# Performance work log

Hardware: AMD Instinct MI355X
Metric: run time of the kernel (lower is better)

The kernel has to match this reference:

```python
import jax, jax.numpy as jnp
import numpy as np

NUM_HEADS = 4
NUM_GROUPS = 8
EPS = 1e-5


def group_norm(x, w, b):
    # x: [B, C, H, W], 8 groups, per-channel affine
    B, C, H, W = x.shape
    g = x.reshape(B, NUM_GROUPS, C // NUM_GROUPS, H, W)
    mu = g.mean(axis=(2, 3, 4), keepdims=True)
    var = g.var(axis=(2, 3, 4), keepdims=True)
    g = (g - mu) * jax.lax.rsqrt(var + EPS)
    x = g.reshape(B, C, H, W)
    return x * w[None, :, None, None] + b[None, :, None, None]


def setup_inputs() -> dict:
    key = jax.random.key(0)
    ks = jax.random.split(key, 7)
    B, C, H, W = 16, 256, 32, 32
    x = jax.random.normal(ks[0], (B, C, H, W), dtype=jnp.float32)
    norm_w = jnp.ones((C,), jnp.float32)
    norm_b = jnp.zeros((C,), jnp.float32)
    # 1x1 convs == channel matmuls; fan-in scaled init
    qkv_w = jax.random.normal(ks[1], (3 * C, C), dtype=jnp.float32) / np.sqrt(C)
    qkv_b = jnp.zeros((3 * C,), jnp.float32)
    proj_w = jax.random.normal(ks[2], (C, C), dtype=jnp.float32) / np.sqrt(C)
    proj_b = jnp.zeros((C,), jnp.float32)
    return {"x": x, "norm_w": norm_w, "norm_b": norm_b,
            "qkv_w": qkv_w, "qkv_b": qkv_b,
            "proj_w": proj_w, "proj_b": proj_b}


def reference(x, norm_w, norm_b, qkv_w, qkv_b, proj_w, proj_b):
    B, C, H, W = x.shape
    nh = NUM_HEADS
    d = C // nh
    N = H * W

    h = group_norm(x, norm_w, norm_b)
    # 1x1 conv -> channel matmul: [B, 3C, H, W]
    qkv = jnp.einsum('oc,bchw->bohw', qkv_w, h) + qkv_b[None, :, None, None]
    qkv = qkv.reshape(B, 3, nh, d, N)
    q, k, v = qkv[:, 0], qkv[:, 1], qkv[:, 2]  # [B, nh, d, N]

    scale = d ** (-0.5)
    attn = jnp.einsum('bhcn,bhcm->bhnm', q, k) * scale  # [B, nh, N, N]
    attn = jax.nn.softmax(attn, axis=-1)
    out = jnp.einsum('bhnm,bhcm->bhcn', attn, v)  # [B, nh, d, N]
    out = out.reshape(B, C, H, W)
    out = jnp.einsum('oc,bchw->bohw', proj_w, out) + proj_b[None, :, None, None]
    return x + out
```

## Files before the change

kernel.cpp:

```cpp
#include <hip/hip_runtime.h>
#include <math.h>

#define BATCH 16
#define CH 256
#define NG 8
#define NH 4
#define HD 64
#define NN 1024
#define GSZ 32
#define GELEMS (GSZ * NN)

typedef __attribute__((ext_vector_type(8))) __bf16 bf16x8;
typedef __attribute__((ext_vector_type(4))) __bf16 bf16x4;
typedef __attribute__((ext_vector_type(4))) float f32x4;

__device__ __forceinline__ unsigned short f2b(float f) {
    union { __bf16 h; unsigned short u; } c; c.h = (__bf16)f; return c.u;
}

#define MFMA(a, b, c) __builtin_amdgcn_mfma_f32_16x16x32_bf16(a, b, c, 0, 0, 0)

typedef __attribute__((address_space(1))) unsigned int ga_u32;
typedef __attribute__((address_space(3))) unsigned int ls_u32;
__device__ __forceinline__ void dma16(const void* g, void* l) {
    __builtin_amdgcn_global_load_lds((ga_u32*)g, (ls_u32*)l, 16, 0, 0);
}

__global__ __launch_bounds__(256) void prep_kernel(
    const float* __restrict__ x, const float* __restrict__ qkv_w,
    const float* __restrict__ proj_w, float* __restrict__ stats,
    unsigned short* __restrict__ wq, unsigned short* __restrict__ wp)
{
    int tid = threadIdx.x;
    if (blockIdx.x >= 128) {
        int t = (blockIdx.x - 128) * 256 + tid;
        const float* src; unsigned short* dst; size_t off;
        if (t < 24576) { src = qkv_w; dst = wq; off = (size_t)t * 8; }
        else           { src = proj_w; dst = wp; off = (size_t)(t - 24576) * 8; }
        const float4* s4 = (const float4*)(src + off);
        float4 a = s4[0], b = s4[1];
        bf16x8 pk;
        pk[0] = (__bf16)a.x; pk[1] = (__bf16)a.y; pk[2] = (__bf16)a.z; pk[3] = (__bf16)a.w;
        pk[4] = (__bf16)b.x; pk[5] = (__bf16)b.y; pk[6] = (__bf16)b.z; pk[7] = (__bf16)b.w;
        *(bf16x8*)(dst + off) = pk;
        return;
    }
    int b = blockIdx.x >> 3, g = blockIdx.x & 7;
    const float4* x4 = (const float4*)(x + ((size_t)b * CH + g * GSZ) * NN);
    float s = 0.f, ss = 0.f;
    #pragma unroll
    for (int i = 0; i < 32; ++i) {
        float4 v = x4[tid + i * 256];
        s  += v.x + v.y + v.z + v.w;
        ss += v.x * v.x + v.y * v.y + v.z * v.z + v.w * v.w;
    }
    #pragma unroll
    for (int off = 1; off < 64; off <<= 1) {
        s  += __shfl_xor(s, off);
        ss += __shfl_xor(ss, off);
    }
    __shared__ float red[8];
    int wave = tid >> 6, lane = tid & 63;
    if (lane == 0) { red[wave] = s; red[4 + wave] = ss; }
    __syncthreads();
    if (tid == 0) {
        float ts  = red[0] + red[1] + red[2] + red[3];
        float tss = red[4] + red[5] + red[6] + red[7];
        float mu  = ts * (1.f / GELEMS);
        float var = tss * (1.f / GELEMS) - mu * mu;
        stats[blockIdx.x * 2] = mu;
        stats[blockIdx.x * 2 + 1] = rsqrtf(var + 1e-5f);
    }
}

__global__ __launch_bounds__(256) void gn_apply_kernel(
    const float* __restrict__ x, const float* __restrict__ w,
    const float* __restrict__ bb, const float* __restrict__ stats,
    unsigned short* __restrict__ hT)
{
    __shared__ float Ts[64][68];
    __shared__ float wcp[256], bcp[256];
    const int b = blockIdx.y, n0 = blockIdx.x * 64;
    const int tid = threadIdx.x;
    {
        int c = tid, g = c >> 5;
        float mu = stats[(b * 8 + g) * 2], rs = stats[(b * 8 + g) * 2 + 1];
        float wc = w[c] * rs;
        wcp[c] = wc; bcp[c] = bb[c] - mu * wc;
    }
    __syncthreads();
    const float* xb = x + (size_t)b * CH * NN;
    const int c_l = tid >> 2, nq = tid & 3;
    const int n_l = tid >> 2, cq = tid & 3;
    for (int cb = 0; cb < 4; ++cb) {
        #pragma unroll
        for (int i = 0; i < 4; ++i)
            *(float4*)&Ts[c_l][nq * 4 + i * 16] =
                *(const float4*)(xb + (size_t)(cb * 64 + c_l) * NN + n0 + nq * 4 + i * 16);
        __syncthreads();
        #pragma unroll
        for (int s = 0; s < 2; ++s) {
            int cbase = cq * 16 + s * 8;
            bf16x8 pk;
            #pragma unroll
            for (int j = 0; j < 8; ++j) {
                int c = cb * 64 + cbase + j;
                pk[j] = (__bf16)(Ts[cbase + j][n_l] * wcp[c] + bcp[c]);
            }
            *(bf16x8*)(hT + ((size_t)b * NN + n0 + n_l) * CH + cb * 64 + cbase) = pk;
        }
        __syncthreads();
    }
}

template <int KIND>
__global__ __launch_bounds__(256) void gemm_kernel(
    const unsigned short* __restrict__ AT,
    const unsigned short* __restrict__ Wb,
    const float* __restrict__ bias,
    unsigned short* __restrict__ outT, unsigned short* __restrict__ outV,
    const float* __restrict__ res, float* __restrict__ out)
{
    __shared__ __align__(16) unsigned short Ws[64][136];
    __shared__ __align__(16) unsigned short Hs[64][136];
    const int b = blockIdx.z, o0 = blockIdx.y * 64, n0 = blockIdx.x * 64;
    const int tid = threadIdx.x;
    const int lane = tid & 63, wv = tid >> 6;
    const int l = lane & 15, quad = lane >> 4;
    const int iw = wv & 1, jw = wv >> 1;
    const bool qk_mode = (KIND == 0) && (blockIdx.y < 8);
    const int r4 = tid >> 2, c4 = tid & 3;

    f32x4 acc[2][2] = {};
    for (int st = 0; st < 2; ++st) {
        const int cc0 = st * 128;
        #pragma unroll
        for (int i = 0; i < 4; ++i) {
            int ch = c4 + i * 4;
            *(bf16x8*)&Ws[r4][ch * 8] =
                *(const bf16x8*)(Wb + (size_t)(o0 + r4) * CH + cc0 + ch * 8);
            *(bf16x8*)&Hs[r4][ch * 8] =
                *(const bf16x8*)(AT + ((size_t)b * NN + n0 + r4) * CH + cc0 + ch * 8);
        }
        __syncthreads();
        #pragma unroll
        for (int kt = 0; kt < 4; ++kt) {
            bf16x8 af[2], bf[2];
            #pragma unroll
            for (int i = 0; i < 2; ++i)
                af[i] = *(const bf16x8*)&Hs[iw * 32 + i * 16 + l][kt * 32 + quad * 8];
            #pragma unroll
            for (int j = 0; j < 2; ++j)
                bf[j] = *(const bf16x8*)&Ws[jw * 32 + j * 16 + l][kt * 32 + quad * 8];
            #pragma unroll
            for (int i = 0; i < 2; ++i)
                #pragma unroll
                for (int j = 0; j < 2; ++j)
                    acc[i][j] = qk_mode ? MFMA(af[i], bf[j], acc[i][j])
                                        : MFMA(bf[j], af[i], acc[i][j]);
        }
        __syncthreads();
    }

    #pragma unroll
    for (int i = 0; i < 2; ++i)
        #pragma unroll
        for (int j = 0; j < 2; ++j) {
            if (qk_mode) {
                int o = o0 + jw * 32 + j * 16 + l;
                float bs = bias[o];
                #pragma unroll
                for (int r = 0; r < 4; ++r) {
                    int n = n0 + iw * 32 + i * 16 + quad * 4 + r;
                    outT[((size_t)b * NN + n) * 512 + o] = f2b(acc[i][j][r] + bs);
                }
            } else {
                int o = o0 + jw * 32 + j * 16 + quad * 4;
                int n = n0 + iw * 32 + i * 16 + l;
                #pragma unroll
                for (int r = 0; r < 4; ++r) {
                    float v = acc[i][j][r] + bias[o + r];
                    if (KIND == 0)
                        outV[((size_t)b * CH + (o + r - 512)) * NN + n] = f2b(v);
                    else {
                        size_t idx = ((size_t)b * CH + o + r) * NN + n;
                        out[idx] = v + res[idx];
                    }
                }
            }
        }
}

__global__ __launch_bounds__(256) void attn_kernel(
    const unsigned short* __restrict__ qkvT,
    const unsigned short* __restrict__ vbuf,
    unsigned short* __restrict__ ctxT)
{
    __shared__ __align__(16) unsigned short KV[8192];
    __shared__ __align__(16) unsigned short Ps[4][32][36];
    __shared__ float Lred[2][2][32];
    const int n0 = blockIdx.x * 64, hh = blockIdx.y, b = blockIdx.z;
    const int tid = threadIdx.x;
    const int lane = tid & 63, w = tid >> 6;
    const int l = lane & 15, quad = lane >> 4;
    const int qx = w & 1, ky = w >> 1;
    const float KL2E = 0.125f * 1.44269504f;

    const int drow = lane >> 3;
    const int dchunk = (lane & 7) ^ (drow & 7);

    bf16x8 qf[2][2];
    {
        const unsigned short* qp = qkvT + ((size_t)b * NN + n0 + 32 * qx + l) * 512 + hh * 64;
        #pragma unroll
        for (int ns = 0; ns < 2; ++ns)
            #pragma unroll
            for (int kt = 0; kt < 2; ++kt)
                qf[ns][kt] = *(const bf16x8*)(qp + (size_t)ns * 16 * 512 + kt * 32 + quad * 8);
    }

    float l_w[2] = {0.f, 0.f};
    f32x4 oacc[2][4] = {};

    for (int mt = 0; mt < 16; ++mt) {
        const int m0 = mt * 64;
        #pragma unroll
        for (int s = 0; s < 2; ++s) {
            int rb = (w * 2 + s) * 8;
            const unsigned short* gk = qkvT + ((size_t)b * NN + m0 + rb + drow) * 512
                                       + 256 + hh * 64 + dchunk * 8;
            dma16(gk, &KV[rb * 64]);
            const unsigned short* gv = vbuf + ((size_t)b * CH + hh * 64 + rb + drow) * NN
                                       + m0 + dchunk * 8;
            dma16(gv, &KV[4096 + rb * 64]);
        }
        __syncthreads();

        f32x4 sacc[2][2] = {};
        #pragma unroll
        for (int kt = 0; kt < 2; ++kt)
            #pragma unroll
            for (int mt2 = 0; mt2 < 2; ++mt2) {
                int r = 32 * ky + 16 * mt2 + l;
                bf16x8 kf = *(const bf16x8*)&KV[r * 64 + (((kt * 4 + quad) ^ (l & 7)) * 8)];
                #pragma unroll
                for (int ns = 0; ns < 2; ++ns)
                    sacc[mt2][ns] = MFMA(kf, qf[ns][kt], sacc[mt2][ns]);
            }

        #pragma unroll
        for (int ns = 0; ns < 2; ++ns)
            #pragma unroll
            for (int mt2 = 0; mt2 < 2; ++mt2) {
                bf16x4 pk;
                #pragma unroll
                for (int r = 0; r < 4; ++r) {
                    float p = exp2f(sacc[mt2][ns][r] * KL2E);
                    l_w[ns] += p;
                    pk[r] = (__bf16)p;
                }
                *(bf16x4*)&Ps[w][ns * 16 + l][mt2 * 16 + quad * 4] = pk;
            }

        #pragma unroll
        for (int ns = 0; ns < 2; ++ns) {
            bf16x8 pa = *(const bf16x8*)&Ps[w][ns * 16 + l][quad * 8];
            #pragma unroll
            for (int ct = 0; ct < 4; ++ct) {
                int r = 16 * ct + l;
                bf16x8 vv = *(const bf16x8*)&KV[4096 + r * 64 + (((ky * 4 + quad) ^ (l & 7)) * 8)];
                oacc[ns][ct] = MFMA(pa, vv, oacc[ns][ct]);
            }
        }
        __syncthreads();
    }

    #pragma unroll
    for (int ns = 0; ns < 2; ++ns) {
        l_w[ns] += __shfl_xor(l_w[ns], 16);
        l_w[ns] += __shfl_xor(l_w[ns], 32);
    }
    __syncthreads();
    float* Ored = (float*)KV;
    if (ky == 1) {
        #pragma unroll
        for (int ns = 0; ns < 2; ++ns) {
            if (quad == 0) Lred[0][qx][ns * 16 + l] = l_w[ns];
            #pragma unroll
            for (int ct = 0; ct < 4; ++ct)
                #pragma unroll
                for (int r = 0; r < 4; ++r)
                    Ored[qx * 2048 + (ns * 16 + quad * 4 + r) * 64 + ct * 16 + l] = oacc[ns][ct][r];
        }
    }
    __syncthreads();
    if (ky == 0) {
        #pragma unroll
        for (int ns = 0; ns < 2; ++ns)
            if (quad == 0)
                Lred[1][qx][ns * 16 + l] = l_w[ns] + Lred[0][qx][ns * 16 + l];
        unsigned short* cb = ctxT + ((size_t)b * NN + n0 + 32 * qx) * CH + hh * 64;
        #pragma unroll
        for (int ns = 0; ns < 2; ++ns) {
            float inv[4];
            #pragma unroll
            for (int r = 0; r < 4; ++r)
                inv[r] = 1.f / Lred[1][qx][ns * 16 + quad * 4 + r];
            #pragma unroll
            for (int ct = 0; ct < 4; ++ct)
                #pragma unroll
                for (int r = 0; r < 4; ++r) {
                    float o = oacc[ns][ct][r] +
                              Ored[qx * 2048 + (ns * 16 + quad * 4 + r) * 64 + ct * 16 + l];
                    cb[(size_t)(ns * 16 + quad * 4 + r) * CH + ct * 16 + l] = f2b(o * inv[r]);
                }
        }
    }
}

extern "C" void kernel_launch(void* const* d_in, const int* in_sizes, int n_in,
                              void* d_out, int out_size, void* d_ws, size_t ws_size,
                              hipStream_t stream)
{
    const float* x      = (const float*)d_in[0];
    const float* norm_w = (const float*)d_in[1];
    const float* norm_b = (const float*)d_in[2];
    const float* qkv_w  = (const float*)d_in[3];
    const float* qkv_b  = (const float*)d_in[4];
    const float* proj_w = (const float*)d_in[5];
    const float* proj_b = (const float*)d_in[6];
    float* out = (float*)d_out;

    unsigned short* hT   = (unsigned short*)d_ws;
    unsigned short* qkvT = hT   + (size_t)BATCH * NN * CH;
    unsigned short* vbuf = qkvT + (size_t)BATCH * NN * 512;
    unsigned short* ctxT = vbuf + (size_t)BATCH * CH * NN;
    unsigned short* wq   = ctxT + (size_t)BATCH * NN * CH;
    unsigned short* wp   = wq + (size_t)768 * CH;
    float* stats         = (float*)(wp + (size_t)CH * CH);

    prep_kernel<<<dim3(256), 256, 0, stream>>>(x, qkv_w, proj_w, stats, wq, wp);
    gn_apply_kernel<<<dim3(16, BATCH), 256, 0, stream>>>(x, norm_w, norm_b, stats, hT);
    gemm_kernel<0><<<dim3(NN / 64, 12, BATCH), 256, 0, stream>>>(
        hT, wq, qkv_b, qkvT, vbuf, nullptr, nullptr);
    attn_kernel<<<dim3(16, NH, BATCH), 256, 0, stream>>>(qkvT, vbuf, ctxT);
    gemm_kernel<1><<<dim3(NN / 64, 4, BATCH), 256, 0, stream>>>(
        ctxT, wp, proj_b, nullptr, nullptr, x, out);
}
```

Before: 156.5 us.

## Load K/V fragments directly from global into registers, drop LDS staging and barriers

The attention kernel no longer stages K and V tiles in shared memory through global_load_lds. Each wave loads its own MFMA K and V fragments straight from global memory into registers, which removes the two __syncthreads per key tile and the KV shared buffer. The grid is flattened to 1D with batch-head as the fast index so that blocks sharing the same K/V are scheduled together for L2 reuse. The Ps row stride also changes. The cost is redundant global/L2 reads, since waves with the same ky fetch identical K/V, and load latency is exposed without explicit double buffering, relying on unroll 2.

```diff
diff --git a/kernel.cpp b/kernel.cpp
--- a/kernel.cpp
+++ b/kernel.cpp
@@ -19,12 +19,6 @@
 }
 
 #define MFMA(a, b, c) __builtin_amdgcn_mfma_f32_16x16x32_bf16(a, b, c, 0, 0, 0)
-
-typedef __attribute__((address_space(1))) unsigned int ga_u32;
-typedef __attribute__((address_space(3))) unsigned int ls_u32;
-__device__ __forceinline__ void dma16(const void* g, void* l) {
-    __builtin_amdgcn_global_load_lds((ga_u32*)g, (ls_u32*)l, 16, 0, 0);
-}
 
 __global__ __launch_bounds__(256) void prep_kernel(
     const float* __restrict__ x, const float* __restrict__ qkv_w,
@@ -196,19 +190,19 @@
     const unsigned short* __restrict__ vbuf,
     unsigned short* __restrict__ ctxT)
 {
-    __shared__ __align__(16) unsigned short KV[8192];
-    __shared__ __align__(16) unsigned short Ps[4][32][36];
+    __shared__ __align__(16) unsigned short Ps[4][32][40];
+    __shared__ float Ored[2][32][64];
     __shared__ float Lred[2][2][32];
-    const int n0 = blockIdx.x * 64, hh = blockIdx.y, b = blockIdx.z;
+    const int id = blockIdx.x;
+    const int bh = id & 63, nt = id >> 6;
+    const int b = bh >> 2, hh = bh & 3;
+    const int n0 = nt * 64;
     const int tid = threadIdx.x;
     const int lane = tid & 63, w = tid >> 6;
     const int l = lane & 15, quad = lane >> 4;
     const int qx = w & 1, ky = w >> 1;
     const float KL2E = 0.125f * 1.44269504f;
 
-    const int drow = lane >> 3;
-    const int dchunk = (lane & 7) ^ (drow & 7);
-
     bf16x8 qf[2][2];
     {
         const unsigned short* qp = qkvT + ((size_t)b * NN + n0 + 32 * qx + l) * 512 + hh * 64;
@@ -218,35 +212,34 @@
             for (int kt = 0; kt < 2; ++kt)
                 qf[ns][kt] = *(const bf16x8*)(qp + (size_t)ns * 16 * 512 + kt * 32 + quad * 8);
     }
+    const unsigned short* kp = qkvT + ((size_t)b * NN + 32 * ky + l) * 512 + 256 + hh * 64
+                               + quad * 8;
+    const unsigned short* vp = vbuf + ((size_t)b * CH + hh * 64 + l) * NN + 32 * ky + quad * 8;
 
     float l_w[2] = {0.f, 0.f};
     f32x4 oacc[2][4] = {};
 
+    #pragma unroll 2
     for (int mt = 0; mt < 16; ++mt) {
         const int m0 = mt * 64;
-        #pragma unroll
-        for (int s = 0; s < 2; ++s) {
-            int rb = (w * 2 + s) * 8;
-            const unsigned short* gk = qkvT + ((size_t)b * NN + m0 + rb + drow) * 512
-                                       + 256 + hh * 64 + dchunk * 8;
-            dma16(gk, &KV[rb * 64]);
-            const unsigned short* gv = vbuf + ((size_t)b * CH + hh * 64 + rb + drow) * NN
-                                       + m0 + dchunk * 8;
-            dma16(gv, &KV[4096 + rb * 64]);
-        }
-        __syncthreads();
+        bf16x8 kf[2][2], vf[4];
+        #pragma unroll
+        for (int mt2 = 0; mt2 < 2; ++mt2)
+            #pragma unroll
+            for (int kt = 0; kt < 2; ++kt)
+                kf[mt2][kt] = *(const bf16x8*)(kp + (size_t)(m0 + 16 * mt2) * 512 + kt * 32);
+        #pragma unroll
+        for (int ct = 0; ct < 4; ++ct)
+            vf[ct] = *(const bf16x8*)(vp + (size_t)(16 * ct) * NN + m0);
 
         f32x4 sacc[2][2] = {};
         #pragma unroll
         for (int kt = 0; kt < 2; ++kt)
             #pragma unroll
-            for (int mt2 = 0; mt2 < 2; ++mt2) {
-                int r = 32 * ky + 16 * mt2 + l;
-                bf16x8 kf = *(const bf16x8*)&KV[r * 64 + (((kt * 4 + quad) ^ (l & 7)) * 8)];
+            for (int mt2 = 0; mt2 < 2; ++mt2)
                 #pragma unroll
                 for (int ns = 0; ns < 2; ++ns)
-                    sacc[mt2][ns] = MFMA(kf, qf[ns][kt], sacc[mt2][ns]);
-            }
+                    sacc[mt2][ns] = MFMA(kf[mt2][kt], qf[ns][kt], sacc[mt2][ns]);
 
         #pragma unroll
         for (int ns = 0; ns < 2; ++ns)
@@ -266,13 +259,9 @@
         for (int ns = 0; ns < 2; ++ns) {
             bf16x8 pa = *(const bf16x8*)&Ps[w][ns * 16 + l][quad * 8];
             #pragma unroll
-            for (int ct = 0; ct < 4; ++ct) {
-                int r = 16 * ct + l;
-                bf16x8 vv = *(const bf16x8*)&KV[4096 + r * 64 + (((ky * 4 + quad) ^ (l & 7)) * 8)];
-                oacc[ns][ct] = MFMA(pa, vv, oacc[ns][ct]);
-            }
-        }
-        __syncthreads();
+            for (int ct = 0; ct < 4; ++ct)
+                oacc[ns][ct] = MFMA(pa, vf[ct], oacc[ns][ct]);
+        }
     }
 
     #pragma unroll
@@ -280,8 +269,6 @@
         l_w[ns] += __shfl_xor(l_w[ns], 16);
         l_w[ns] += __shfl_xor(l_w[ns], 32);
     }
-    __syncthreads();
-    float* Ored = (float*)KV;
     if (ky == 1) {
         #pragma unroll
         for (int ns = 0; ns < 2; ++ns) {
@@ -290,7 +277,7 @@
             for (int ct = 0; ct < 4; ++ct)
                 #pragma unroll
                 for (int r = 0; r < 4; ++r)
-                    Ored[qx * 2048 + (ns * 16 + quad * 4 + r) * 64 + ct * 16 + l] = oacc[ns][ct][r];
+                    Ored[qx][ns * 16 + quad * 4 + r][ct * 16 + l] = oacc[ns][ct][r];
         }
     }
     __syncthreads();
@@ -311,7 +298,7 @@
                 #pragma unroll
                 for (int r = 0; r < 4; ++r) {
                     float o = oacc[ns][ct][r] +
-                              Ored[qx * 2048 + (ns * 16 + quad * 4 + r) * 64 + ct * 16 + l];
+                              Ored[qx][ns * 16 + quad * 4 + r][ct * 16 + l];
                     cb[(size_t)(ns * 16 + quad * 4 + r) * CH + ct * 16 + l] = f2b(o * inv[r]);
                 }
         }
@@ -343,7 +330,7 @@
     gn_apply_kernel<<<dim3(16, BATCH), 256, 0, stream>>>(x, norm_w, norm_b, stats, hT);
     gemm_kernel<0><<<dim3(NN / 64, 12, BATCH), 256, 0, stream>>>(
         hT, wq, qkv_b, qkvT, vbuf, nullptr, nullptr);
-    attn_kernel<<<dim3(16, NH, BATCH), 256, 0, stream>>>(qkvT, vbuf, ctxT);
+    attn_kernel<<<dim3(1024), 256, 0, stream>>>(qkvT, vbuf, ctxT);
     gemm_kernel<1><<<dim3(NN / 64, 4, BATCH), 256, 0, stream>>>(
         ctxT, wp, proj_b, nullptr, nullptr, x, out);
 }
```

Measured after the change: 179.7 us. +14.8%, slower.
